# Kernel optimization log

Hardware: AMD Instinct MI355X
Metric: run time of the kernel (lower is better)

Reference implementation:

```python
import jax, jax.numpy as jnp
import numpy as np

EPS = 1e-6


def setup_inputs() -> dict:
    key = jax.random.key(0)
    kx, ky = jax.random.split(key)
    B, C, H, W = 8, 128, 48, 64
    x = jax.random.normal(kx, (B, C, H, W), dtype=jnp.float32)
    y = jax.random.normal(ky, (B, C, H, W), dtype=jnp.float32)
    return {"x": x, "y": y}


def reference(x, y):
    # x, y: (b, c, h, w)
    b, c, h, w = x.shape
    # torch: x.transpose(2,3).view(b,c,h*w) -> x flattened w-major,
    #        so output channel k = v*h + u corresponds to x[:, :, u, v].
    # corr5[b, v, u, i, j] = sum_c x[b,c,u,v] * y[b,c,i,j]
    corr = jnp.einsum('bcuv,bcij->bvuij', x, y)
    corr = corr.reshape(b, w * h, h, w)  # channel k = v*h + u
    # normalization: ReLU then L2-normalize over the h*w channel dim
    corr = jax.nn.relu(corr)
    norm = jnp.sqrt(jnp.sum(corr * corr, axis=1, keepdims=True) + EPS)
    return corr / norm
```

## Files before the change

kernel.cpp:

```cpp
#include <hip/hip_runtime.h>
#include <hip/hip_bf16.h>

#define NB 8
#define NC 128
#define NH 48
#define NW 64
#define NS 3072
#define EPSF 1e-6f

#define GLOBAL_AS __attribute__((address_space(1)))
#define LDS_AS __attribute__((address_space(3)))

typedef __bf16 bf16x8 __attribute__((ext_vector_type(8)));
typedef float f32x4 __attribute__((ext_vector_type(4)));

__global__ __launch_bounds__(256) void transpose_both(
    const float* __restrict__ x, const float* __restrict__ y,
    __hip_bfloat16* __restrict__ AT, __hip_bfloat16* __restrict__ BT) {
  __shared__ float tile[32][65];
  const int id = blockIdx.x;
  const int b = id & 7;
  const int which = (id >> 3) & 1;
  const int rr = id >> 4;
  const int f0 = (rr % 96) * 32, c0 = (rr / 96) * 64;
  const float* src = which ? y : x;
  __hip_bfloat16* dst = which ? BT : AT;
  const int t = threadIdx.x;

  const int fi = t & 31, ci0 = t >> 5;
  const float* sp = src + ((size_t)b * NC + c0) * NS + f0;
#pragma unroll
  for (int i = 0; i < 8; ++i) {
    int ci = ci0 + i * 8;
    tile[fi][ci] = sp[(size_t)ci * NS + fi];
  }
  __syncthreads();

  const int co = t & 63, fo0 = t >> 6;
#pragma unroll
  for (int i = 0; i < 8; ++i) {
    int fo = fo0 + i * 4;
    int f = f0 + fo;
    int k = which ? f : ((f & 63) * NH + (f >> 6));
    dst[((size_t)b * NS + k) * NC + c0 + co] = __float2bfloat16(tile[fo][co]);
  }
}

template <bool WRITE>
__global__ __launch_bounds__(256, 2) void corr_gemm(
    const __hip_bfloat16* __restrict__ AT,
    const __hip_bfloat16* __restrict__ BT,
    const float* __restrict__ part_in, float* __restrict__ part_out,
    float* __restrict__ out) {
  __shared__ char smem[66560];
  float* rnc = (float*)(smem + 65536);
  const int id = blockIdx.x;
  const int b = id & 7;
  const int tl = id >> 3;
  const int mt = tl / 24, nt = tl - mt * 24;
  const int t = threadIdx.x;
  const int lane = t & 63, wid = t >> 6;
  const int wm = wid >> 1, wn = wid & 1;
  const int l15 = lane & 15, kg = lane >> 4;

  const char* Ag = (const char*)(AT + ((size_t)b * NS + mt * 128) * NC);
  const char* Bg = (const char*)(BT + ((size_t)b * NS + nt * 128) * NC);
  {
    const int lr = lane >> 4, lg = lane & 15;
#pragma unroll
    for (int i = 0; i < 8; ++i) {
      int c = wid * 8 + i;
      int row = c * 4 + lr;
      int g = lg ^ (row & 7);
      int go = row * 256 + g * 16;
      __builtin_amdgcn_global_load_lds((const GLOBAL_AS unsigned*)(Ag + go),
                                       (LDS_AS unsigned*)(smem + c * 1024),
                                       16, 0, 0);
      __builtin_amdgcn_global_load_lds(
          (const GLOBAL_AS unsigned*)(Bg + go),
          (LDS_AS unsigned*)(smem + 32768 + c * 1024), 16, 0, 0);
    }
  }
  if (WRITE) {
    if (t < 128) {
      float s = 0.f;
#pragma unroll
      for (int q = 0; q < 24; ++q)
        s += part_in[(size_t)q * (NB * NS) + (size_t)b * NS + nt * 128 + t];
      rnc[t] = rsqrtf(s + EPSF);
    }
  }
  __syncthreads();

  f32x4 acc[4][4] = {};
  const int rx = l15 & 7;
#pragma unroll
  for (int kk = 0; kk < 4; ++kk) {
    int g = (kk * 4 + kg) ^ rx;
    bf16x8 a[4], bb[4];
#pragma unroll
    for (int mi = 0; mi < 4; ++mi) {
      int row = wm * 64 + mi * 16 + l15;
      a[mi] = *(const bf16x8*)(smem + row * 256 + g * 16);
    }
#pragma unroll
    for (int ni = 0; ni < 4; ++ni) {
      int row = wn * 64 + ni * 16 + l15;
      bb[ni] = *(const bf16x8*)(smem + 32768 + row * 256 + g * 16);
    }
#pragma unroll
    for (int mi = 0; mi < 4; ++mi)
#pragma unroll
      for (int ni = 0; ni < 4; ++ni)
        acc[mi][ni] = __builtin_amdgcn_mfma_f32_16x16x32_bf16(
            a[mi], bb[ni], acc[mi][ni], 0, 0, 0);
  }

  if (!WRITE) {
    float cs[4] = {0.f, 0.f, 0.f, 0.f};
#pragma unroll
    for (int ni = 0; ni < 4; ++ni)
#pragma unroll
      for (int mi = 0; mi < 4; ++mi)
#pragma unroll
        for (int r = 0; r < 4; ++r) {
          float v = fmaxf(acc[mi][ni][r], 0.f);
          cs[ni] += v * v;
        }
#pragma unroll
    for (int ni = 0; ni < 4; ++ni) {
      cs[ni] += __shfl_xor(cs[ni], 16, 64);
      cs[ni] += __shfl_xor(cs[ni], 32, 64);
    }
    __syncthreads();
    float* csum = (float*)smem;
    if (kg == 0) {
#pragma unroll
      for (int ni = 0; ni < 4; ++ni)
        csum[wm * 128 + wn * 64 + ni * 16 + l15] = cs[ni];
    }
    __syncthreads();
    if (t < 128) {
      float s = csum[t] + csum[128 + t];
      part_out[(size_t)mt * (NB * NS) + (size_t)b * NS + nt * 128 + t] = s;
    }
  } else {
    float rnv[4];
#pragma unroll
    for (int ni = 0; ni < 4; ++ni) rnv[ni] = rnc[wn * 64 + ni * 16 + l15];
    __syncthreads();

    float* tf = (float*)smem;
#pragma unroll
    for (int mi = 0; mi < 4; ++mi)
#pragma unroll
      for (int ni = 0; ni < 4; ++ni)
#pragma unroll
        for (int r = 0; r < 4; ++r) {
          int row = wm * 64 + mi * 16 + kg * 4 + r;
          int col = wn * 64 + ni * 16 + l15;
          tf[row * 129 + col] = fmaxf(acc[mi][ni][r], 0.f) * rnv[ni];
        }
    __syncthreads();

    float* ob = out + (size_t)b * NS * NS + (size_t)(mt * 128) * NS + nt * 128;
    const int rsub = t >> 5, c4 = (t & 31) * 4;
#pragma unroll
    for (int it = 0; it < 16; ++it) {
      int row = it * 8 + rsub;
      f32x4 v = *(const f32x4*)&tf[row * 129 + c4];
      __builtin_nontemporal_store(v, (f32x4*)&ob[(size_t)row * NS + c4]);
    }
  }
}

extern "C" void kernel_launch(void* const* d_in, const int* in_sizes, int n_in,
                              void* d_out, int out_size, void* d_ws,
                              size_t ws_size, hipStream_t stream) {
  const float* x = (const float*)d_in[0];
  const float* y = (const float*)d_in[1];
  float* out = (float*)d_out;
  char* ws = (char*)d_ws;

  const size_t AT_OFF = 0;
  const size_t BT_OFF = 6291456;
  const size_t PART_OFF = 12582912;
  const size_t NEED = 14942208;
  if (ws_size < NEED) return;

  __hip_bfloat16* AT = (__hip_bfloat16*)(ws + AT_OFF);
  __hip_bfloat16* BT = (__hip_bfloat16*)(ws + BT_OFF);
  float* part = (float*)(ws + PART_OFF);

  dim3 tb(256);
  transpose_both<<<dim3(3072), tb, 0, stream>>>(x, y, AT, BT);
  corr_gemm<false><<<dim3(4608), tb, 0, stream>>>(AT, BT, nullptr, part,
                                                  nullptr);
  corr_gemm<true><<<dim3(4608), tb, 0, stream>>>(AT, BT, part, nullptr, out);
}
```

Before: 99.85 us.

## Replace partial-sum norm pass with per-column-tile looping kernel

```diff
diff --git a/kernel.cpp b/kernel.cpp
--- a/kernel.cpp
+++ b/kernel.cpp
@@ -46,11 +46,106 @@
   }
 }
 
-template <bool WRITE>
-__global__ __launch_bounds__(256, 2) void corr_gemm(
+__device__ __forceinline__ void stage_tile(const char* gsrc, char* ldst,
+                                           int wid, int lane) {
+  const int lr = lane >> 4, lg = lane & 15;
+#pragma unroll
+  for (int i = 0; i < 8; ++i) {
+    int c = wid * 8 + i;
+    int row = c * 4 + lr;
+    int g = lg ^ (row & 7);
+    __builtin_amdgcn_global_load_lds(
+        (const GLOBAL_AS unsigned*)(gsrc + row * 256 + g * 16),
+        (LDS_AS unsigned*)(ldst + c * 1024), 16, 0, 0);
+  }
+}
+
+__device__ __forceinline__ void gemm_step(const char* As, const char* Bs,
+                                          float cs[4], int wm, int wn,
+                                          int l15, int kg) {
+  f32x4 acc[4][4] = {};
+  const int rx = l15 & 7;
+#pragma unroll
+  for (int kk = 0; kk < 4; ++kk) {
+    int g = (kk * 4 + kg) ^ rx;
+    bf16x8 a[4], bb[4];
+#pragma unroll
+    for (int mi = 0; mi < 4; ++mi)
+      a[mi] = *(const bf16x8*)(As + (wm * 64 + mi * 16 + l15) * 256 + g * 16);
+#pragma unroll
+    for (int ni = 0; ni < 4; ++ni)
+      bb[ni] = *(const bf16x8*)(Bs + (wn * 64 + ni * 16 + l15) * 256 + g * 16);
+#pragma unroll
+    for (int mi = 0; mi < 4; ++mi)
+#pragma unroll
+      for (int ni = 0; ni < 4; ++ni)
+        acc[mi][ni] = __builtin_amdgcn_mfma_f32_16x16x32_bf16(
+            a[mi], bb[ni], acc[mi][ni], 0, 0, 0);
+  }
+#pragma unroll
+  for (int ni = 0; ni < 4; ++ni)
+#pragma unroll
+    for (int mi = 0; mi < 4; ++mi)
+#pragma unroll
+      for (int r = 0; r < 4; ++r) {
+        float v = fmaxf(acc[mi][ni][r], 0.f);
+        cs[ni] += v * v;
+      }
+}
+
+__global__ __launch_bounds__(256, 1) void corr_norm(
     const __hip_bfloat16* __restrict__ AT,
-    const __hip_bfloat16* __restrict__ BT,
-    const float* __restrict__ part_in, float* __restrict__ part_out,
+    const __hip_bfloat16* __restrict__ BT, float* __restrict__ rn) {
+  __shared__ char smem[98304];
+  char* Bs = smem + 65536;
+  const int id = blockIdx.x;
+  const int b = id & 7;
+  const int nt = id >> 3;
+  const int t = threadIdx.x;
+  const int lane = t & 63, wid = t >> 6;
+  const int wm = wid >> 1, wn = wid & 1;
+  const int l15 = lane & 15, kg = lane >> 4;
+
+  const char* Ab = (const char*)(AT + (size_t)b * NS * NC);
+  const char* Bg = (const char*)(BT + ((size_t)b * NS + nt * 128) * NC);
+
+  stage_tile(Bg, Bs, wid, lane);
+  stage_tile(Ab, smem, wid, lane);
+  __syncthreads();
+
+  float cs[4] = {0.f, 0.f, 0.f, 0.f};
+#pragma unroll 1
+  for (int mt = 0; mt < 24; mt += 2) {
+    stage_tile(Ab + (size_t)(mt + 1) * 32768, smem + 32768, wid, lane);
+    gemm_step(smem, Bs, cs, wm, wn, l15, kg);
+    __syncthreads();
+    if (mt + 2 < 24)
+      stage_tile(Ab + (size_t)(mt + 2) * 32768, smem, wid, lane);
+    gemm_step(smem + 32768, Bs, cs, wm, wn, l15, kg);
+    __syncthreads();
+  }
+
+#pragma unroll
+  for (int ni = 0; ni < 4; ++ni) {
+    cs[ni] += __shfl_xor(cs[ni], 16, 64);
+    cs[ni] += __shfl_xor(cs[ni], 32, 64);
+  }
+  float* csum = (float*)smem;
+  if (kg == 0) {
+#pragma unroll
+    for (int ni = 0; ni < 4; ++ni)
+      csum[wm * 128 + wn * 64 + ni * 16 + l15] = cs[ni];
+  }
+  __syncthreads();
+  if (t < 128) {
+    float s = csum[t] + csum[128 + t];
+    rn[(size_t)b * NS + nt * 128 + t] = rsqrtf(s + EPSF);
+  }
+}
+
+__global__ __launch_bounds__(256, 2) void corr_out(
+    const __hip_bfloat16* __restrict__ AT,
+    const __hip_bfloat16* __restrict__ BT, const float* __restrict__ rn,
     float* __restrict__ out) {
   __shared__ char smem[66560];
   float* rnc = (float*)(smem + 65536);
@@ -65,31 +160,9 @@
 
   const char* Ag = (const char*)(AT + ((size_t)b * NS + mt * 128) * NC);
   const char* Bg = (const char*)(BT + ((size_t)b * NS + nt * 128) * NC);
-  {
-    const int lr = lane >> 4, lg = lane & 15;
-#pragma unroll
-    for (int i = 0; i < 8; ++i) {
-      int c = wid * 8 + i;
-      int row = c * 4 + lr;
-      int g = lg ^ (row & 7);
-      int go = row * 256 + g * 16;
-      __builtin_amdgcn_global_load_lds((const GLOBAL_AS unsigned*)(Ag + go),
-                                       (LDS_AS unsigned*)(smem + c * 1024),
-                                       16, 0, 0);
-      __builtin_amdgcn_global_load_lds(
-          (const GLOBAL_AS unsigned*)(Bg + go),
-          (LDS_AS unsigned*)(smem + 32768 + c * 1024), 16, 0, 0);
-    }
-  }
-  if (WRITE) {
-    if (t < 128) {
-      float s = 0.f;
-#pragma unroll
-      for (int q = 0; q < 24; ++q)
-        s += part_in[(size_t)q * (NB * NS) + (size_t)b * NS + nt * 128 + t];
-      rnc[t] = rsqrtf(s + EPSF);
-    }
-  }
+  stage_tile(Ag, smem, wid, lane);
+  stage_tile(Bg, smem + 32768, wid, lane);
+  if (t < 128) rnc[t] = rn[(size_t)b * NS + nt * 128 + t];
   __syncthreads();
 
   f32x4 acc[4][4] = {};
@@ -99,15 +172,12 @@
     int g = (kk * 4 + kg) ^ rx;
     bf16x8 a[4], bb[4];
 #pragma unroll
-    for (int mi = 0; mi < 4; ++mi) {
-      int row = wm * 64 + mi * 16 + l15;
-      a[mi] = *(const bf16x8*)(smem + row * 256 + g * 16);
-    }
-#pragma unroll
-    for (int ni = 0; ni < 4; ++ni) {
-      int row = wn * 64 + ni * 16 + l15;
-      bb[ni] = *(const bf16x8*)(smem + 32768 + row * 256 + g * 16);
-    }
+    for (int mi = 0; mi < 4; ++mi)
+      a[mi] = *(const bf16x8*)(smem + (wm * 64 + mi * 16 + l15) * 256 + g * 16);
+#pragma unroll
+    for (int ni = 0; ni < 4; ++ni)
+      bb[ni] = *(const bf16x8*)(smem + 32768 +
+                                (wn * 64 + ni * 16 + l15) * 256 + g * 16);
 #pragma unroll
     for (int mi = 0; mi < 4; ++mi)
 #pragma unroll
@@ -116,61 +186,31 @@
             a[mi], bb[ni], acc[mi][ni], 0, 0, 0);
   }
 
-  if (!WRITE) {
-    float cs[4] = {0.f, 0.f, 0.f, 0.f};
-#pragma unroll
-    for (int ni = 0; ni < 4; ++ni)
-#pragma unroll
-      for (int mi = 0; mi < 4; ++mi)
-#pragma unroll
-        for (int r = 0; r < 4; ++r) {
-          float v = fmaxf(acc[mi][ni][r], 0.f);
-          cs[ni] += v * v;
-        }
-#pragma unroll
-    for (int ni = 0; ni < 4; ++ni) {
-      cs[ni] += __shfl_xor(cs[ni], 16, 64);
-      cs[ni] += __shfl_xor(cs[ni], 32, 64);
-    }
-    __syncthreads();
-    float* csum = (float*)smem;
-    if (kg == 0) {
-#pragma unroll
-      for (int ni = 0; ni < 4; ++ni)
-        csum[wm * 128 + wn * 64 + ni * 16 + l15] = cs[ni];
-    }
-    __syncthreads();
-    if (t < 128) {
-      float s = csum[t] + csum[128 + t];
-      part_out[(size_t)mt * (NB * NS) + (size_t)b * NS + nt * 128 + t] = s;
-    }
-  } else {
-    float rnv[4];
-#pragma unroll
-    for (int ni = 0; ni < 4; ++ni) rnv[ni] = rnc[wn * 64 + ni * 16 + l15];
-    __syncthreads();
-
-    float* tf = (float*)smem;
-#pragma unroll
-    for (int mi = 0; mi < 4; ++mi)
-#pragma unroll
-      for (int ni = 0; ni < 4; ++ni)
-#pragma unroll
-        for (int r = 0; r < 4; ++r) {
-          int row = wm * 64 + mi * 16 + kg * 4 + r;
-          int col = wn * 64 + ni * 16 + l15;
-          tf[row * 129 + col] = fmaxf(acc[mi][ni][r], 0.f) * rnv[ni];
-        }
-    __syncthreads();
-
-    float* ob = out + (size_t)b * NS * NS + (size_t)(mt * 128) * NS + nt * 128;
-    const int rsub = t >> 5, c4 = (t & 31) * 4;
-#pragma unroll
-    for (int it = 0; it < 16; ++it) {
-      int row = it * 8 + rsub;
-      f32x4 v = *(const f32x4*)&tf[row * 129 + c4];
-      __builtin_nontemporal_store(v, (f32x4*)&ob[(size_t)row * NS + c4]);
-    }
+  float rnv[4];
+#pragma unroll
+  for (int ni = 0; ni < 4; ++ni) rnv[ni] = rnc[wn * 64 + ni * 16 + l15];
+  __syncthreads();
+
+  float* tf = (float*)smem;
+#pragma unroll
+  for (int mi = 0; mi < 4; ++mi)
+#pragma unroll
+    for (int ni = 0; ni < 4; ++ni)
+#pragma unroll
+      for (int r = 0; r < 4; ++r) {
+        int row = wm * 64 + mi * 16 + kg * 4 + r;
+        int col = wn * 64 + ni * 16 + l15;
+        tf[row * 129 + col] = fmaxf(acc[mi][ni][r], 0.f) * rnv[ni];
+      }
+  __syncthreads();
+
+  float* ob = out + (size_t)b * NS * NS + (size_t)(mt * 128) * NS + nt * 128;
+  const int rsub = t >> 5, c4 = (t & 31) * 4;
+#pragma unroll
+  for (int it = 0; it < 16; ++it) {
+    int row = it * 8 + rsub;
+    f32x4 v = *(const f32x4*)&tf[row * 129 + c4];
+    __builtin_nontemporal_store(v, (f32x4*)&ob[(size_t)row * NS + c4]);
   }
 }
 
@@ -184,17 +224,16 @@
 
   const size_t AT_OFF = 0;
   const size_t BT_OFF = 6291456;
-  const size_t PART_OFF = 12582912;
-  const size_t NEED = 14942208;
+  const size_t RN_OFF = 12582912;
+  const size_t NEED = 12681216;
   if (ws_size < NEED) return;
 
   __hip_bfloat16* AT = (__hip_bfloat16*)(ws + AT_OFF);
   __hip_bfloat16* BT = (__hip_bfloat16*)(ws + BT_OFF);
-  float* part = (float*)(ws + PART_OFF);
+  float* rn = (float*)(ws + RN_OFF);
 
   dim3 tb(256);
   transpose_both<<<dim3(3072), tb, 0, stream>>>(x, y, AT, BT);
-  corr_gemm<false><<<dim3(4608), tb, 0, stream>>>(AT, BT, nullptr, part,
-                                                  nullptr);
-  corr_gemm<true><<<dim3(4608), tb, 0, stream>>>(AT, BT, part, nullptr, out);
-}
+  corr_norm<<<dim3(192), tb, 0, stream>>>(AT, BT, rn);
+  corr_out<<<dim3(4608), tb, 0, stream>>>(AT, BT, rn, out);
+}
```

Result: slower. 102.4 us (+2.5%).
